# Kernel optimization log

Measured on AMD Instinct MI355X. Metric: run time of the kernel, lower is better.

Reference implementation:

```python
import jax, jax.numpy as jnp
import numpy as np

# Model/config dims
N_NODE = 500000   # num_node (item vocab)
D      = 100      # opt.hiddenSize
B      = 512      # batch
S      = 50       # session seq len
NS     = 12       # opt.n_sample neighbors per node
HOP    = 1        # opt.n_iter
STEP   = 1        # opt.step (star-graph propagation steps)
LAST   = 3        # opt.last_len
NADJ   = 12       # adjacent items per last item
SCALE  = 1.0 / np.sqrt(D)


def setup_inputs() -> dict:
    key = jax.random.key(0)
    ks = jax.random.split(key, 16)
    stdv = 1.0 / np.sqrt(D)
    u = lambda k, sh: jax.random.uniform(k, sh, jnp.float32, -stdv, stdv)
    return {
        # forward args
        "inputs":     jax.random.randint(ks[0], (B, S), 0, N_NODE),
        "adj":        jax.random.uniform(ks[1], (B, S, S), jnp.float32),
        "item":       jax.random.randint(ks[2], (B, S), 0, N_NODE),
        "last_items": jax.random.randint(ks[3], (B, LAST), 0, N_NODE),
        "adj_items":  jax.random.randint(ks[4], (B, LAST * NADJ), 0, N_NODE),
        # learned params / buffers
        "embedding": u(ks[5], (N_NODE, D)),
        "s":         u(ks[6], (2, 1)),
        "W_star_a":  u(ks[7], (D, D)),
        "W_star_q":  u(ks[8], (D, D)),
        "W_star_k":  u(ks[9], (D, D)),
        "W_g":       u(ks[10], (2 * D, D)),
        "W_l":       u(ks[11], (D, D)),
        "adj_all":   jax.random.randint(ks[12], (N_NODE, NS), 0, N_NODE),
        "num_w":     jax.random.uniform(ks[13], (N_NODE, NS), jnp.float32),
    }


def _l2norm(x):
    # F.normalize(p=2, dim=-1)
    return x / jnp.maximum(jnp.linalg.norm(x, axis=-1, keepdims=True), 1e-12)


def reference(inputs, adj, item, last_items, adj_items,
              embedding, s, W_star_a, W_star_q, W_star_k, W_g, W_l,
              adj_all, num_w):
    # ----- embedding lookup + padding mask -----
    h = embedding[inputs]                                  # [B,S,D]
    mask = (inputs != 0).astype(h.dtype)                   # [B,S]

    # ----- StarAggregator (local branch): star node + gated propagation -----
    denom = jnp.maximum(mask.sum(-1, keepdims=True), 1.0)
    star = (h * mask[..., None]).sum(1) / denom            # [B,D] masked mean
    hl = h
    for _ in range(STEP):
        h_n = jnp.einsum('bst,btd->bsd', adj, hl @ W_star_a)          # neighbor agg
        gate = jax.nn.sigmoid(
            jnp.einsum('bsd,bd->bs', hl @ W_star_q, star @ W_star_k) * SCALE)
        hl = (1.0 - gate)[..., None] * h_n + gate[..., None] * star[:, None, :]
        beta = jnp.einsum('bsd,bd->bs', hl, star) * SCALE
        beta = jax.nn.softmax(jnp.where(mask > 0, beta, -1e9), axis=1)
        star = jnp.einsum('bs,bsd->bd', beta, hl)
    h_local = hl                                           # [B,S,D]

    # ----- GlobalAggregator (hop=1 neighbor-sampling branch) -----
    flat = inputs.reshape(-1)
    neigh_idx = adj_all[flat].reshape(B, S, NS)            # gathered neighbor ids
    neigh_w = num_w[flat].reshape(B, S, NS)                # co-occurrence weights
    neigh = embedding[neigh_idx]                           # [B,S,NS,D]
    alpha = jax.nn.softmax(neigh_w, axis=-1)
    agg = jnp.einsum('bsn,bsnd->bsd', alpha, neigh)        # weighted neighbor sum
    h_global = jax.nn.relu(jnp.concatenate([h, agg], -1) @ W_g)  # [B,S,D]

    # ----- normalize + (eval-mode dropout = identity) + learned 2-way combine -----
    h_local = _l2norm(h_local)
    h_global = _l2norm(h_global)
    output = jnp.einsum('bsdk,ko->bsdo',
                        jnp.stack([h_local, h_global], axis=-1), s)[..., 0]  # [B,S,D]

    # ----- LastAggregator (last-items attention branch) -----
    item_h = embedding[last_items]                         # [B,L,D]
    adj_h = embedding[adj_items].reshape(B, LAST, -1, D)   # [B,L,NADJ,D]
    q = item_h @ W_l
    att = jax.nn.softmax(jnp.einsum('bld,blnd->bln', q, adj_h) * SCALE, axis=-1)
    aggl = jnp.einsum('bln,blnd->bld', att, adj_h)
    last_hidden = (item_h + aggl).mean(axis=1)             # [B,D]

    return output, last_hidden
```

## Files before the change

### kernel.cpp

```cpp
#include <hip/hip_runtime.h>
#include <hip/hip_fp16.h>

#define B_    512
#define S_    50
#define D_    100
#define NS_   12
#define LAST_ 3
#define NADJ_ 12
#define SCALE_ 0.1f

#define GEMM_STEP(ACC, BUF, K, W0, W1, W2, W3)                                      \
    _Pragma("unroll")                                                                \
    for (int i = 0; i < 5; ++i) {                                                    \
        float4 x = *(const float4*)&BUF[sb + i][K];                                  \
        ACC[i][0] = fmaf(x.x,W0.x, fmaf(x.y,W1.x, fmaf(x.z,W2.x, fmaf(x.w,W3.x, ACC[i][0])))); \
        ACC[i][1] = fmaf(x.x,W0.y, fmaf(x.y,W1.y, fmaf(x.z,W2.y, fmaf(x.w,W3.y, ACC[i][1])))); \
        ACC[i][2] = fmaf(x.x,W0.z, fmaf(x.y,W1.z, fmaf(x.z,W2.z, fmaf(x.w,W3.z, ACC[i][2])))); \
        ACC[i][3] = fmaf(x.x,W0.w, fmaf(x.y,W1.w, fmaf(x.z,W2.w, fmaf(x.w,W3.w, ACC[i][3])))); \
    }

__global__ __launch_bounds__(256, 3) void fused_all(
    const int* __restrict__ inputs,
    const float* __restrict__ adj,
    const float* __restrict__ emb,
    const int* __restrict__ adj_all,
    const float* __restrict__ num_w,
    const float* __restrict__ sW,
    const float* __restrict__ Wa,
    const float* __restrict__ Wq,
    const float* __restrict__ Wk,
    const float* __restrict__ Wg,
    const int* __restrict__ last_items,
    const int* __restrict__ adj_items,
    const float* __restrict__ Wl,
    float* __restrict__ out)
{
    __shared__ __align__(16) float hL[S_][D_];
    __shared__ __align__(16) float hwa[S_][D_];
    __shared__ __align__(16) union UAS {
        __half adjH[S_][S_];
        float  ssq[S_][25];
    } u;
    __shared__ float star[D_], kb[D_], kq[D_];
    __shared__ float gate[S_], rinv[S_], rinv2[S_];
    __shared__ int   ids[S_];
    __shared__ int   nid[S_ * NS_];
    __shared__ float alf[S_ * NS_];
    __shared__ float denom;

    const int t = threadIdx.x;

    if (blockIdx.x >= B_) {
        const int b = blockIdx.x - B_;
        float* ih  = &hL[0][0];
        float* ah  = &hL[0][0] + 304;
        float* qL  = &hwa[0][0];
        float* att = &u.ssq[0][0];
        int*   li  = ids;
        int*   ai  = nid;

        if (t < LAST_) li[t] = last_items[b * LAST_ + t];
        if (t < LAST_ * NADJ_) ai[t] = adj_items[b * LAST_ * NADJ_ + t];
        __syncthreads();

        for (int e = t; e < LAST_ * 25; e += 256) {
            int l = e / 25, dq = e - l * 25;
            ((float4*)ih)[e] = ((const float4*)(emb + li[l] * D_))[dq];
        }
        for (int e = t; e < LAST_ * NADJ_ * 25; e += 256) {
            int j = e / 25, dq = e - j * 25;
            ((float4*)ah)[e] = ((const float4*)(emb + ai[j] * D_))[dq];
        }
        __syncthreads();

        for (int e = t; e < LAST_ * D_; e += 256) {
            int l = e / D_, d = e - l * D_;
            float a = 0.f;
            for (int k = 0; k < D_; ++k) a = fmaf(ih[l * D_ + k], Wl[k * D_ + d], a);
            qL[e] = a;
        }
        __syncthreads();

        if (t < LAST_ * NADJ_) {
            int l = t / NADJ_;
            const float* ar = ah + t * D_;
            const float* qr = qL + l * D_;
            float a = 0.f;
            for (int d = 0; d < D_; ++d) a = fmaf(qr[d], ar[d], a);
            att[t] = a * SCALE_;
        }
        __syncthreads();

        if (t < LAST_) {
            float mx = -1e30f;
            for (int n = 0; n < NADJ_; ++n) mx = fmaxf(mx, att[t * NADJ_ + n]);
            float ex[NADJ_]; float sm = 0.f;
            for (int n = 0; n < NADJ_; ++n) { ex[n] = __expf(att[t * NADJ_ + n] - mx); sm += ex[n]; }
            float inv = 1.f / sm;
            for (int n = 0; n < NADJ_; ++n) att[t * NADJ_ + n] = ex[n] * inv;
        }
        __syncthreads();

        if (t < D_) {
            float acc = 0.f;
            for (int l = 0; l < LAST_; ++l) {
                float a = ih[l * D_ + t];
                for (int n = 0; n < NADJ_; ++n)
                    a = fmaf(att[l * NADJ_ + n], ah[(l * NADJ_ + n) * D_ + t], a);
                acc += a;
            }
            out[B_ * S_ * D_ + b * D_ + t] = acc * (1.f / 3.f);
        }
        return;
    }

    const int b = blockIdx.x;
    const float s0 = sW[0], s1 = sW[1];

    const bool act = (t < 250);
    int sg = 0, dg = 0, sb = 0, d4 = 0;
    if (act) { sg = t / 25; dg = t - sg * 25; sb = sg * 5; d4 = dg * 4; }

    const float4* WaQ = (const float4*)Wa;
    float4 wa0, wa1, wa2, wa3;
    if (act) {
        wa0 = WaQ[0 * 25 + dg]; wa1 = WaQ[1 * 25 + dg];
        wa2 = WaQ[2 * 25 + dg]; wa3 = WaQ[3 * 25 + dg];
    }

    if (t < S_) ids[t] = inputs[b * S_ + t];
    __syncthreads();

    if (t < 64) {
        unsigned long long m = __ballot(t < S_ && ids[t] != 0);
        if (t == 0) denom = fmaxf((float)__popcll(m), 1.f);
    }
    for (int e = t; e < S_ * 25; e += 256) {
        int s = e / 25, dq = e - s * 25;
        ((float4*)&hL[0][0])[e] = ((const float4*)(emb + ids[s] * D_))[dq];
    }
    {
        __half2* dst = (__half2*)&u.adjH[0][0];
        const float4* src = (const float4*)(adj + b * S_ * S_);
        for (int e = t; e < S_ * S_ / 4; e += 256) {
            float4 v = src[e];
            dst[2 * e]     = __floats2half2_rn(v.x, v.y);
            dst[2 * e + 1] = __floats2half2_rn(v.z, v.w);
        }
    }
    for (int e = t; e < S_ * NS_; e += 256) {
        int r = e / NS_, n = e - r * NS_;
        nid[e] = adj_all[ids[r] * NS_ + n];
        alf[e] = num_w[ids[r] * NS_ + n];
    }
    __syncthreads();

    if (t < D_) {
        float a = 0.f;
        for (int s = 0; s < S_; ++s) a += (ids[s] != 0) ? hL[s][t] : 0.f;
        star[t] = a / denom;
    } else if (t >= 128 && t < 128 + S_) {
        int r = t - 128;
        float mx = -1e30f;
#pragma unroll
        for (int n = 0; n < NS_; ++n) mx = fmaxf(mx, alf[r * NS_ + n]);
        float ex[NS_]; float sm = 0.f;
#pragma unroll
        for (int n = 0; n < NS_; ++n) { ex[n] = __expf(alf[r * NS_ + n] - mx); sm += ex[n]; }
        float inv = 1.f / sm;
#pragma unroll
        for (int n = 0; n < NS_; ++n) alf[r * NS_ + n] = ex[n] * inv;
    }
    __syncthreads();

    if (t < D_) {
        float a = 0.f;
        for (int k = 0; k < D_; ++k) a = fmaf(star[k], Wk[k * D_ + t], a);
        kb[t] = a;
    }
    __syncthreads();

    if (t < D_) {
        float a = 0.f;
        const float4* wr = (const float4*)(Wq + t * D_);
#pragma unroll 5
        for (int j = 0; j < 25; ++j) {
            float4 uq = wr[j]; int k = j * 4;
            a = fmaf(uq.x, kb[k + 0], a); a = fmaf(uq.y, kb[k + 1], a);
            a = fmaf(uq.z, kb[k + 2], a); a = fmaf(uq.w, kb[k + 3], a);
        }
        kq[t] = a;
    }
    __syncthreads();

    if (t < S_) {
        float a = 0.f;
        const float4* hr = (const float4*)&hL[t][0];
#pragma unroll 5
        for (int j = 0; j < 25; ++j) {
            float4 uq = hr[j]; int k = j * 4;
            a = fmaf(uq.x, kq[k + 0], a); a = fmaf(uq.y, kq[k + 1], a);
            a = fmaf(uq.z, kq[k + 2], a); a = fmaf(uq.w, kq[k + 3], a);
        }
        gate[t] = 1.f / (1.f + __expf(-a * SCALE_));
    }

    if (act) {
        float acc[5][4] = {};
        for (int k = 0; k < 96; k += 4) {
            float4 n0 = WaQ[(k + 4) * 25 + dg], n1 = WaQ[(k + 5) * 25 + dg],
                   n2 = WaQ[(k + 6) * 25 + dg], n3 = WaQ[(k + 7) * 25 + dg];
            GEMM_STEP(acc, hL, k, wa0, wa1, wa2, wa3)
            wa0 = n0; wa1 = n1; wa2 = n2; wa3 = n3;
        }
        GEMM_STEP(acc, hL, 96, wa0, wa1, wa2, wa3)
#pragma unroll
        for (int i = 0; i < 5; ++i) {
            float4 v; v.x = acc[i][0]; v.y = acc[i][1]; v.z = acc[i][2]; v.w = acc[i][3];
            *(float4*)&hwa[sb + i][d4] = v;
        }
    }
    __syncthreads();

    float hl[5][4] = {};
    if (act) {
        for (int k = 0; k < S_; k += 2) {
            float4 w0 = *(const float4*)&hwa[k][d4];
            float4 w1 = *(const float4*)&hwa[k + 1][d4];
#pragma unroll
            for (int i = 0; i < 5; ++i) {
                float2 a2 = __half22float2(*(const __half2*)&u.adjH[sb + i][k]);
                hl[i][0] = fmaf(a2.x, w0.x, fmaf(a2.y, w1.x, hl[i][0]));
                hl[i][1] = fmaf(a2.x, w0.y, fmaf(a2.y, w1.y, hl[i][1]));
                hl[i][2] = fmaf(a2.x, w0.z, fmaf(a2.y, w1.z, hl[i][2]));
                hl[i][3] = fmaf(a2.x, w0.w, fmaf(a2.y, w1.w, hl[i][3]));
            }
        }
#pragma unroll
        for (int i = 0; i < 5; ++i) {
            float g = gate[sb + i];
#pragma unroll
            for (int j = 0; j < 4; ++j)
                hl[i][j] = (1.f - g) * hl[i][j] + g * star[d4 + j];
        }
    }
    __syncthreads();

    const float4* WgQ = (const float4*)Wg;
    float4 wg0, wg1, wg2, wg3;
    if (act) {
        wg0 = WgQ[0 * 25 + dg]; wg1 = WgQ[1 * 25 + dg];
        wg2 = WgQ[2 * 25 + dg]; wg3 = WgQ[3 * 25 + dg];
#pragma unroll
        for (int i = 0; i < 5; ++i)
            u.ssq[sb + i][dg] = hl[i][0]*hl[i][0] + hl[i][1]*hl[i][1]
                              + hl[i][2]*hl[i][2] + hl[i][3]*hl[i][3];
#pragma unroll
        for (int i = 0; i < 5; ++i) {
            int row = sb + i;
            float a0 = 0.f, a1 = 0.f, a2 = 0.f, a3 = 0.f;
#pragma unroll
            for (int n = 0; n < NS_; ++n) {
                float4 uq = ((const float4*)(emb + nid[row * NS_ + n] * D_))[dg];
                float al = alf[row * NS_ + n];
                a0 = fmaf(al, uq.x, a0); a1 = fmaf(al, uq.y, a1);
                a2 = fmaf(al, uq.z, a2); a3 = fmaf(al, uq.w, a3);
            }
            float4 v; v.x = a0; v.y = a1; v.z = a2; v.w = a3;
            *(float4*)&hwa[row][d4] = v;
        }
    }
    __syncthreads();

    if (t < S_) {
        float ss = 0.f;
#pragma unroll
        for (int j = 0; j < 25; ++j) ss += u.ssq[t][j];
        rinv[t] = s0 / fmaxf(sqrtf(ss), 1e-12f);
    }
    __syncthreads();

    float o[5][4] = {};
    if (act) {
#pragma unroll
        for (int i = 0; i < 5; ++i) {
            float f = rinv[sb + i];
#pragma unroll
            for (int j = 0; j < 4; ++j) hl[i][j] *= f;
        }
        for (int k = 0; k < 96; k += 4) {
            float4 n0 = WgQ[(k + 4) * 25 + dg], n1 = WgQ[(k + 5) * 25 + dg],
                   n2 = WgQ[(k + 6) * 25 + dg], n3 = WgQ[(k + 7) * 25 + dg];
            GEMM_STEP(o, hL, k, wg0, wg1, wg2, wg3)
            wg0 = n0; wg1 = n1; wg2 = n2; wg3 = n3;
        }
        {
            float4 n0 = WgQ[100 * 25 + dg], n1 = WgQ[101 * 25 + dg],
                   n2 = WgQ[102 * 25 + dg], n3 = WgQ[103 * 25 + dg];
            GEMM_STEP(o, hL, 96, wg0, wg1, wg2, wg3)
            wg0 = n0; wg1 = n1; wg2 = n2; wg3 = n3;
        }
        for (int k = 0; k < 96; k += 4) {
            float4 n0 = WgQ[(100 + k + 4) * 25 + dg], n1 = WgQ[(100 + k + 5) * 25 + dg],
                   n2 = WgQ[(100 + k + 6) * 25 + dg], n3 = WgQ[(100 + k + 7) * 25 + dg];
            GEMM_STEP(o, hwa, k, wg0, wg1, wg2, wg3)
            wg0 = n0; wg1 = n1; wg2 = n2; wg3 = n3;
        }
        GEMM_STEP(o, hwa, 96, wg0, wg1, wg2, wg3)
#pragma unroll
        for (int i = 0; i < 5; ++i) {
#pragma unroll
            for (int j = 0; j < 4; ++j) o[i][j] = fmaxf(o[i][j], 0.f);
            u.ssq[sb + i][dg] = o[i][0]*o[i][0] + o[i][1]*o[i][1]
                              + o[i][2]*o[i][2] + o[i][3]*o[i][3];
        }
    }
    __syncthreads();

    if (t < S_) {
        float ss = 0.f;
#pragma unroll
        for (int j = 0; j < 25; ++j) ss += u.ssq[t][j];
        rinv2[t] = s1 / fmaxf(sqrtf(ss), 1e-12f);
    }
    __syncthreads();

    if (act) {
#pragma unroll
        for (int i = 0; i < 5; ++i) {
            float f = rinv2[sb + i];
            int row = b * S_ + sb + i;
            float4 ov;
            ov.x = hl[i][0] + o[i][0] * f;
            ov.y = hl[i][1] + o[i][1] * f;
            ov.z = hl[i][2] + o[i][2] * f;
            ov.w = hl[i][3] + o[i][3] * f;
            ((float4*)(out + row * D_))[dg] = ov;
        }
    }
}

extern "C" void kernel_launch(void* const* d_in, const int* in_sizes, int n_in,
                              void* d_out, int out_size, void* d_ws, size_t ws_size,
                              hipStream_t stream) {
    (void)in_sizes; (void)n_in; (void)out_size; (void)d_ws; (void)ws_size;
    const int* inputs     = (const int*)d_in[0];
    const float* adj      = (const float*)d_in[1];
    const int* last_items = (const int*)d_in[3];
    const int* adj_items  = (const int*)d_in[4];
    const float* emb      = (const float*)d_in[5];
    const float* sW       = (const float*)d_in[6];
    const float* Wa       = (const float*)d_in[7];
    const float* Wq       = (const float*)d_in[8];
    const float* Wk       = (const float*)d_in[9];
    const float* Wg       = (const float*)d_in[10];
    const float* Wl       = (const float*)d_in[11];
    const int* adj_all    = (const int*)d_in[12];
    const float* num_w    = (const float*)d_in[13];

    float* out = (float*)d_out;

    fused_all<<<2 * B_, 256, 0, stream>>>(inputs, adj, emb, adj_all, num_w,
                                          sW, Wa, Wq, Wk, Wg,
                                          last_items, adj_items, Wl, out);
}
```

Baseline: 353.4 us.

## Software-pipeline neighbor embedding gathers across stages and use nontemporal memory ops

The 12-neighbor embedding gather for each of the 5 rows is split into issue and consume steps. These are interleaved with the star, key/query, gate, Wa GEMM and propagation stages, so the gather latency is hidden behind other work. The neighbor softmax moves into each thread's consume step, which recomputes it redundantly per thread. Embedding, adj loads and output stores also become nontemporal loads and stores. The cost is more live registers (12 float4 in flight plus the aggregates) under launch bounds 256,3, which may cause spills.

After: 343.7 us. 1.03x faster.

```diff
diff --git a/kernel.cpp b/kernel.cpp
--- a/kernel.cpp
+++ b/kernel.cpp
@@ -8,6 +8,12 @@
 #define LAST_ 3
 #define NADJ_ 12
 #define SCALE_ 0.1f
+
+typedef __attribute__((ext_vector_type(4))) float f4;
+
+__device__ __forceinline__ f4 ntload4(const float* p) {
+    return __builtin_nontemporal_load((const f4*)p);
+}
 
 #define GEMM_STEP(ACC, BUF, K, W0, W1, W2, W3)                                      \
     _Pragma("unroll")                                                                \
@@ -17,6 +23,31 @@
         ACC[i][1] = fmaf(x.x,W0.y, fmaf(x.y,W1.y, fmaf(x.z,W2.y, fmaf(x.w,W3.y, ACC[i][1])))); \
         ACC[i][2] = fmaf(x.x,W0.z, fmaf(x.y,W1.z, fmaf(x.z,W2.z, fmaf(x.w,W3.z, ACC[i][2])))); \
         ACC[i][3] = fmaf(x.x,W0.w, fmaf(x.y,W1.w, fmaf(x.z,W2.w, fmaf(x.w,W3.w, ACC[i][3])))); \
+    }
+
+#define AGG_ISSUE(I)                                                                 \
+    {   int base = (sb + (I)) * NS_;                                                 \
+        _Pragma("unroll")                                                            \
+        for (int n = 0; n < NS_; ++n)                                                \
+            q[n] = ntload4(emb + nid[base + n] * D_ + d4);                           \
+    }
+#define AGG_CONSUME(I)                                                               \
+    {   int base = (sb + (I)) * NS_;                                                 \
+        float mx = -1e30f;                                                           \
+        _Pragma("unroll")                                                            \
+        for (int n = 0; n < NS_; ++n) mx = fmaxf(mx, alf[base + n]);                 \
+        float agw[NS_]; float sm = 0.f;                                              \
+        _Pragma("unroll")                                                            \
+        for (int n = 0; n < NS_; ++n) { agw[n] = __expf(alf[base + n] - mx); sm += agw[n]; } \
+        float inv = 1.f / sm;                                                        \
+        _Pragma("unroll")                                                            \
+        for (int n = 0; n < NS_; ++n) {                                              \
+            float w = agw[n] * inv;                                                  \
+            agg[I][0] = fmaf(w, q[n].x, agg[I][0]);                                  \
+            agg[I][1] = fmaf(w, q[n].y, agg[I][1]);                                  \
+            agg[I][2] = fmaf(w, q[n].z, agg[I][2]);                                  \
+            agg[I][3] = fmaf(w, q[n].w, agg[I][3]);                                  \
+        }                                                                            \
     }
 
 __global__ __launch_bounds__(256, 3) void fused_all(
@@ -65,11 +96,11 @@
 
         for (int e = t; e < LAST_ * 25; e += 256) {
             int l = e / 25, dq = e - l * 25;
-            ((float4*)ih)[e] = ((const float4*)(emb + li[l] * D_))[dq];
+            ((f4*)ih)[e] = ntload4(emb + li[l] * D_ + dq * 4);
         }
         for (int e = t; e < LAST_ * NADJ_ * 25; e += 256) {
             int j = e / 25, dq = e - j * 25;
-            ((float4*)ah)[e] = ((const float4*)(emb + ai[j] * D_))[dq];
+            ((f4*)ah)[e] = ntload4(emb + ai[j] * D_ + dq * 4);
         }
         __syncthreads();
 
@@ -109,7 +140,8 @@
                     a = fmaf(att[l * NADJ_ + n], ah[(l * NADJ_ + n) * D_ + t], a);
                 acc += a;
             }
-            out[B_ * S_ * D_ + b * D_ + t] = acc * (1.f / 3.f);
+            __builtin_nontemporal_store(acc * (1.f / 3.f),
+                                        out + B_ * S_ * D_ + b * D_ + t);
         }
         return;
     }
@@ -137,13 +169,13 @@
     }
     for (int e = t; e < S_ * 25; e += 256) {
         int s = e / 25, dq = e - s * 25;
-        ((float4*)&hL[0][0])[e] = ((const float4*)(emb + ids[s] * D_))[dq];
+        ((f4*)&hL[0][0])[e] = ntload4(emb + ids[s] * D_ + dq * 4);
     }
     {
         __half2* dst = (__half2*)&u.adjH[0][0];
-        const float4* src = (const float4*)(adj + b * S_ * S_);
+        const float* src = adj + b * S_ * S_;
         for (int e = t; e < S_ * S_ / 4; e += 256) {
-            float4 v = src[e];
+            f4 v = ntload4(src + e * 4);
             dst[2 * e]     = __floats2half2_rn(v.x, v.y);
             dst[2 * e + 1] = __floats2half2_rn(v.z, v.w);
         }
@@ -155,21 +187,14 @@
     }
     __syncthreads();
 
+    f4 q[NS_];
+    float agg[5][4] = {};
+
+    if (act) AGG_ISSUE(0)
     if (t < D_) {
         float a = 0.f;
         for (int s = 0; s < S_; ++s) a += (ids[s] != 0) ? hL[s][t] : 0.f;
         star[t] = a / denom;
-    } else if (t >= 128 && t < 128 + S_) {
-        int r = t - 128;
-        float mx = -1e30f;
-#pragma unroll
-        for (int n = 0; n < NS_; ++n) mx = fmaxf(mx, alf[r * NS_ + n]);
-        float ex[NS_]; float sm = 0.f;
-#pragma unroll
-        for (int n = 0; n < NS_; ++n) { ex[n] = __expf(alf[r * NS_ + n] - mx); sm += ex[n]; }
-        float inv = 1.f / sm;
-#pragma unroll
-        for (int n = 0; n < NS_; ++n) alf[r * NS_ + n] = ex[n] * inv;
     }
     __syncthreads();
 
@@ -178,6 +203,7 @@
         for (int k = 0; k < D_; ++k) a = fmaf(star[k], Wk[k * D_ + t], a);
         kb[t] = a;
     }
+    if (act) { AGG_CONSUME(0) AGG_ISSUE(1) }
     __syncthreads();
 
     if (t < D_) {
@@ -191,6 +217,7 @@
         }
         kq[t] = a;
     }
+    if (act) { AGG_CONSUME(1) AGG_ISSUE(2) }
     __syncthreads();
 
     if (t < S_) {
@@ -204,8 +231,8 @@
         }
         gate[t] = 1.f / (1.f + __expf(-a * SCALE_));
     }
-
-    if (act) {
+    if (act) {
+        AGG_CONSUME(2)
         float acc[5][4] = {};
         for (int k = 0; k < 96; k += 4) {
             float4 n0 = WaQ[(k + 4) * 25 + dg], n1 = WaQ[(k + 5) * 25 + dg],
@@ -219,6 +246,7 @@
             float4 v; v.x = acc[i][0]; v.y = acc[i][1]; v.z = acc[i][2]; v.w = acc[i][3];
             *(float4*)&hwa[sb + i][d4] = v;
         }
+        AGG_ISSUE(3)
     }
     __syncthreads();
 
@@ -243,6 +271,7 @@
             for (int j = 0; j < 4; ++j)
                 hl[i][j] = (1.f - g) * hl[i][j] + g * star[d4 + j];
         }
+        AGG_CONSUME(3) AGG_ISSUE(4)
     }
     __syncthreads();
 
@@ -251,23 +280,15 @@
     if (act) {
         wg0 = WgQ[0 * 25 + dg]; wg1 = WgQ[1 * 25 + dg];
         wg2 = WgQ[2 * 25 + dg]; wg3 = WgQ[3 * 25 + dg];
+        AGG_CONSUME(4)
 #pragma unroll
         for (int i = 0; i < 5; ++i)
             u.ssq[sb + i][dg] = hl[i][0]*hl[i][0] + hl[i][1]*hl[i][1]
                               + hl[i][2]*hl[i][2] + hl[i][3]*hl[i][3];
 #pragma unroll
         for (int i = 0; i < 5; ++i) {
-            int row = sb + i;
-            float a0 = 0.f, a1 = 0.f, a2 = 0.f, a3 = 0.f;
-#pragma unroll
-            for (int n = 0; n < NS_; ++n) {
-                float4 uq = ((const float4*)(emb + nid[row * NS_ + n] * D_))[dg];
-                float al = alf[row * NS_ + n];
-                a0 = fmaf(al, uq.x, a0); a1 = fmaf(al, uq.y, a1);
-                a2 = fmaf(al, uq.z, a2); a3 = fmaf(al, uq.w, a3);
-            }
-            float4 v; v.x = a0; v.y = a1; v.z = a2; v.w = a3;
-            *(float4*)&hwa[row][d4] = v;
+            float4 v; v.x = agg[i][0]; v.y = agg[i][1]; v.z = agg[i][2]; v.w = agg[i][3];
+            *(float4*)&hwa[sb + i][d4] = v;
         }
     }
     __syncthreads();
@@ -330,12 +351,12 @@
         for (int i = 0; i < 5; ++i) {
             float f = rinv2[sb + i];
             int row = b * S_ + sb + i;
-            float4 ov;
+            f4 ov;
             ov.x = hl[i][0] + o[i][0] * f;
             ov.y = hl[i][1] + o[i][1] * f;
             ov.z = hl[i][2] + o[i][2] * f;
             ov.w = hl[i][3] + o[i][3] * f;
-            ((float4*)(out + row * D_))[dg] = ov;
+            __builtin_nontemporal_store(ov, (f4*)(out + row * D_) + dg);
         }
     }
 }
```
